# Kernel optimization log

Measured on AMD Instinct MI355X. Metric: run time of the kernel, lower is better.

## Reference

```python
import jax, jax.numpy as jnp
import numpy as np

B, M, S, N, DIN, C = 2048, 5, 128, 128, 64, 32
MID = C // 2  # 16
EPS = 1e-5
NEG_SLOPE = 0.2


def setup_inputs() -> dict:
    key = jax.random.key(0)
    ks = jax.random.split(key, 13)
    sc = lambda fan: 1.0 / np.sqrt(fan)
    return {
        "x_global": jax.random.normal(ks[0], (B, N, C), jnp.float32),
        "x_local": jax.random.normal(ks[1], (B * M, S, DIN), jnp.float32),
        "W_lin": jax.random.normal(ks[2], (C, DIN), jnp.float32) * sc(DIN),
        "b_lin": jnp.zeros((C,), jnp.float32),
        "W_att": jax.random.normal(ks[3], (C,), jnp.float32) * sc(C),  # Conv2d(C,1,1) weight
        "Wa": jax.random.normal(ks[4], (MID, C), jnp.float32) * sc(C),
        "Wb": jax.random.normal(ks[5], (MID, C), jnp.float32) * sc(C),
        "Wc": jax.random.normal(ks[6], (MID, C), jnp.float32) * sc(C),
        "Wn": jax.random.normal(ks[7], (MID, MID), jnp.float32) * sc(MID),
        "Wl": jax.random.normal(ks[8], (MID, MID), jnp.float32) * sc(MID),
        "Wd": jax.random.normal(ks[9], (C, 2 * MID), jnp.float32) * sc(2 * MID),
        "bn_gamma": jnp.ones((C,), jnp.float32),
        "bn_beta": jnp.zeros((C,), jnp.float32),
    }


def reference(x_global, x_local, W_lin, b_lin, W_att, Wa, Wb, Wc, Wn, Wl, Wd, bn_gamma, bn_beta):
    # --- Motion_Aggregation_Module.forward ---
    xl = x_local.reshape(B, M, S, DIN)
    xl = jnp.einsum('bmsd,cd->bmsc', xl, W_lin) + b_lin          # Linear(64,32)
    curves = jnp.transpose(xl, (0, 3, 1, 2))                      # [B,C,M,S]
    x = jnp.transpose(x_global, (0, 2, 1))                        # [B,C,N]

    # --- Correlation_Module.forward ---
    att = jnp.einsum('c,bcms->bms', W_att, curves)                # line_conv_att -> [B,M,S]
    inter = jnp.einsum('bcms,bms->bcm', curves, jax.nn.softmax(att, axis=-1))  # [B,C,M]
    intra = jnp.einsum('bcms,bms->bcs', curves, jax.nn.softmax(att, axis=-2))  # [B,C,S]

    inter = jnp.einsum('oc,bcm->bom', Wa, inter)                  # conva -> [B,MID,M]
    intra = jnp.einsum('oc,bcs->bos', Wb, intra)                  # convb -> [B,MID,S]
    x_logits = jnp.einsum('oc,bcn->bno', Wc, x)                   # convc^T -> [B,N,MID]

    a_inter = jax.nn.softmax(jnp.einsum('bno,bom->bnm', x_logits, inter), axis=-1)  # [B,N,M]
    a_intra = jax.nn.softmax(jnp.einsum('bno,bos->bns', x_logits, intra), axis=-1)  # [B,N,S]

    v_inter = jnp.einsum('po,bom->bmp', Wn, inter)                # convn^T -> [B,M,MID]
    v_intra = jnp.einsum('po,bos->bsp', Wl, intra)                # convl^T -> [B,S,MID]

    f_inter = jnp.einsum('bnm,bmp->bnp', a_inter, v_inter)        # [B,N,MID]
    f_intra = jnp.einsum('bns,bsp->bnp', a_intra, v_intra)        # [B,N,MID]
    feat = jnp.concatenate([f_inter, f_intra], axis=-1)           # [B,N,2*MID]
    feat = jnp.einsum('oc,bnc->bon', Wd, feat)                    # convd conv -> [B,C,N]

    # BatchNorm1d (training mode: batch stats over (B, N), biased variance)
    mean = feat.mean(axis=(0, 2), keepdims=True)
    var = feat.var(axis=(0, 2), keepdims=True)
    feat = (feat - mean) * jax.lax.rsqrt(var + EPS)
    feat = feat * bn_gamma[None, :, None] + bn_beta[None, :, None]

    out = x + feat                                                # residual
    out = jnp.where(out >= 0, out, NEG_SLOPE * out)               # leaky_relu(0.2)
    return jnp.transpose(out, (0, 2, 1))                          # [B,N,C]
```

## Files before the change

kernel.cpp:

```cpp
#include <hip/hip_runtime.h>
#include <math.h>

#define NB 2048
typedef float f32x4 __attribute__((ext_vector_type(4)));
typedef float f32x2 __attribute__((ext_vector_type(2)));

#define P_WAL 0
#define P_WBL 1024
#define P_WLBL 2048
#define P_WNAL 3072
#define P_WEFF 4096
#define P_BWA 4160
#define P_BWB 4176
#define P_BWL 4192
#define P_BWN 4208
#define P_C0  4224

#define WS_BNPART 4352
#define WS_COEF   135424
#define WS_SMALL  135488
#define WS_BIG_I  463168
#define WS_BIG_V  (463168 + 4194304)
#define WS_FEAT16 (463168 + 8388608)

__device__ __forceinline__ unsigned short f2bf(float f) {
  unsigned int u = __float_as_uint(f);
  u += 0x7fffu + ((u >> 16) & 1u);
  return (unsigned short)(u >> 16);
}
__device__ __forceinline__ unsigned int pack2bf(float lo, float hi) {
  return (unsigned int)f2bf(lo) | ((unsigned int)f2bf(hi) << 16);
}
__device__ __forceinline__ float bflo(unsigned int u) { return __uint_as_float(u << 16); }
__device__ __forceinline__ float bfhi(unsigned int u) { return __uint_as_float(u & 0xffff0000u); }

#define BSTAGE(MASK, HALF)                                        \
  { const bool hi_ = (lane & (MASK)) != 0;                        \
    _Pragma("unroll")                                             \
    for (int k_ = 0; k_ < (HALF); ++k_) {                         \
      float mine_ = hi_ ? a[k_ + (HALF)] : a[k_];                 \
      float oth_  = hi_ ? a[k_] : a[k_ + (HALF)];                 \
      a[k_] = mine_ + __shfl_xor(oth_, (MASK));                   \
    } }

__global__ __launch_bounds__(256) void k0_pre(const float* __restrict__ W_lin,
                                              const float* __restrict__ b_lin,
                                              const float* __restrict__ W_att,
                                              const float* __restrict__ Wa,
                                              const float* __restrict__ Wb,
                                              const float* __restrict__ Wn,
                                              const float* __restrict__ Wl,
                                              float* __restrict__ pre) {
  int t = threadIdx.x;
  for (int i = t; i < 1024; i += 256) {
    int o = i >> 6, d = i & 63;
    float sa = 0.f, sb = 0.f;
    for (int c = 0; c < 32; ++c) {
      float wl = W_lin[c * 64 + d];
      sa += Wa[o * 32 + c] * wl;
      sb += Wb[o * 32 + c] * wl;
    }
    pre[P_WAL + i] = sa;
    pre[P_WBL + i] = sb;
  }
  if (t < 64) {
    float s = 0.f;
    for (int c = 0; c < 32; ++c) s += W_att[c] * W_lin[c * 64 + t];
    pre[P_WEFF + t] = s;
  }
  if (t < 16) {
    float sa = 0.f, sb = 0.f;
    for (int c = 0; c < 32; ++c) {
      sa += Wa[t * 32 + c] * b_lin[c];
      sb += Wb[t * 32 + c] * b_lin[c];
    }
    pre[P_BWA + t] = sa;
    pre[P_BWB + t] = sb;
  }
  if (t == 0) {
    float s = 0.f;
    for (int c = 0; c < 32; ++c) s += W_att[c] * b_lin[c];
    pre[P_C0] = s;
  }
  __syncthreads();
  for (int i = t; i < 1024; i += 256) {
    int p_ = i >> 6, d = i & 63;
    float sl = 0.f, sn = 0.f;
    for (int o = 0; o < 16; ++o) {
      sl += Wl[p_ * 16 + o] * pre[P_WBL + o * 64 + d];
      sn += Wn[p_ * 16 + o] * pre[P_WAL + o * 64 + d];
    }
    pre[P_WLBL + i] = sl;
    pre[P_WNAL + i] = sn;
  }
  if (t < 16) {
    float sl = 0.f, sn = 0.f;
    for (int o = 0; o < 16; ++o) {
      sl += Wl[t * 16 + o] * pre[P_BWB + o];
      sn += Wn[t * 16 + o] * pre[P_BWA + o];
    }
    pre[P_BWL + t] = sl;
    pre[P_BWN + t] = sn;
  }
}

__global__ __launch_bounds__(1024, 2) void k1a(
    const float* __restrict__ xl_all, const float* __restrict__ pre,
    float* __restrict__ p_small, float* __restrict__ bigI,
    float* __restrict__ bigV) {
  __shared__ __align__(16) float xaggi[128 * 68];
  __shared__ f32x4 scratch5[5][16][16];
  __shared__ float pe[5][16];
  __shared__ float xagg_inter[5][64];

  const int t = threadIdx.x;
  const int b = blockIdx.x;
  const int lane = t & 63;
  const int w = t >> 6;
  const int q = lane >> 4;
  const int i16 = lane & 15;

  const float* xl = xl_all + (size_t)b * (5 * 128 * 64);
  const f32x4 weff4 = ((const f32x4*)(pre + P_WEFF))[i16];
  const float c0 = pre[P_C0];

  const float* xb = xl + (size_t)(8 * w + q) * 64 + 4 * i16;

  f32x4 xA[2], xB[2], acc[2];
  float Zk[2];
  #pragma unroll
  for (int k = 0; k < 2; ++k) {
    acc[k] = (f32x4)0.f;
    Zk[k] = 0.f;
    xA[k] = *(const f32x4*)(xb + k * 256);
  }

  #pragma unroll
  for (int m = 0; m < 5; ++m) {
    f32x4* xc = (m & 1) ? xB : xA;
    f32x4* xn = (m & 1) ? xA : xB;
    if (m < 4) {
      const float* np = xb + (size_t)(m + 1) * 8192;
      #pragma unroll
      for (int k = 0; k < 2; ++k) xn[k] = *(const f32x4*)(np + k * 256);
    }
    float a0, a1;
    {
      f32x4 p0 = xc[0] * weff4, p1 = xc[1] * weff4;
      a0 = p0.x + p0.y + p0.z + p0.w;
      a1 = p1.x + p1.y + p1.z + p1.w;
    }
    #pragma unroll
    for (int mask = 1; mask <= 8; mask <<= 1) {
      a0 += __shfl_xor(a0, mask);
      a1 += __shfl_xor(a1, mask);
    }
    float e0 = __expf(a0 + c0), e1 = __expf(a1 + c0);
    Zk[0] += e0; Zk[1] += e1;
    f32x4 pim;
    {
      f32x4 pr0 = e0 * xc[0];
      f32x4 pr1 = e1 * xc[1];
      acc[0] += pr0; acc[1] += pr1;
      pim = pr0 + pr1;
    }
    float se = e0 + e1;
    #pragma unroll
    for (int mask = 16; mask <= 32; mask <<= 1) {
      pim.x += __shfl_xor(pim.x, mask);
      pim.y += __shfl_xor(pim.y, mask);
      pim.z += __shfl_xor(pim.z, mask);
      pim.w += __shfl_xor(pim.w, mask);
      se += __shfl_xor(se, mask);
    }
    if (lane < 16) {
      scratch5[m][w][i16] = pim;
      if (i16 == 0) pe[m][w] = se;
    }
  }

  #pragma unroll
  for (int k = 0; k < 2; ++k) {
    float invz = 1.f / Zk[k];
    f32x4 v = acc[k] * invz;
    int r = 8 * w + 4 * k + q;
    *(f32x4*)&xaggi[r * 68 + 4 * i16] = v;
  }
  __syncthreads();

  if (t < 320) {
    int mm = t >> 6, d = t & 63;
    const float* sp = (const float*)&scratch5[mm][0][0];
    float s = 0.f;
    #pragma unroll
    for (int j = 0; j < 16; ++j) s += sp[j * 64 + d];
    float sume = 0.f;
    #pragma unroll
    for (int j = 0; j < 16; ++j) sume += pe[mm][j];
    xagg_inter[mm][d] = s / sume;
  }
  __syncthreads();

  if (t < 512) {
    const int q2 = __builtin_amdgcn_readfirstlane(t >> 7);
    const int s2 = t & 127;
    const float* Wbase = pre + ((q2 < 2) ? P_WBL : P_WLBL) + (q2 & 1) * 512;
    const float* xrow = &xaggi[s2 * 68];
    float acc2[8];
    #pragma unroll
    for (int r = 0; r < 8; ++r) acc2[r] = 0.f;
    #pragma unroll
    for (int c = 0; c < 64; c += 4) {
      f32x4 xa = *(const f32x4*)(xrow + c);
      #pragma unroll
      for (int r = 0; r < 8; ++r)
        acc2[r] += xa.x * Wbase[r * 64 + c] + xa.y * Wbase[r * 64 + c + 1] +
                   xa.z * Wbase[r * 64 + c + 2] + xa.w * Wbase[r * 64 + c + 3];
    }
    const int bb = ((q2 < 2) ? P_BWB : P_BWL) + (q2 & 1) * 8;
    float* dst = ((q2 < 2) ? bigI : bigV) + (size_t)b * 2048 + s2 * 16 + (q2 & 1) * 8;
    f32x4 o0, o1;
    o0.x = acc2[0] + pre[bb + 0];
    o0.y = acc2[1] + pre[bb + 1];
    o0.z = acc2[2] + pre[bb + 2];
    o0.w = acc2[3] + pre[bb + 3];
    o1.x = acc2[4] + pre[bb + 4];
    o1.y = acc2[5] + pre[bb + 5];
    o1.z = acc2[6] + pre[bb + 6];
    o1.w = acc2[7] + pre[bb + 7];
    *(f32x4*)dst = o0;
    *(f32x4*)(dst + 4) = o1;
  } else if (t < 672) {
    int tt = t - 512;
    int o2 = tt & 31, mm = tt >> 5;
    const float* wr = pre + ((o2 < 16) ? (P_WAL + o2 * 64) : (P_WNAL + (o2 - 16) * 64));
    float p = 0.f;
    #pragma unroll
    for (int d = 0; d < 64; ++d) p += wr[d] * xagg_inter[mm][d];
    p += (o2 < 16) ? pre[P_BWA + o2] : pre[P_BWN + (o2 - 16)];
    float* os = p_small + (size_t)b * 160;
    if (o2 < 16) os[mm * 16 + o2] = p;
    else os[80 + mm * 16 + (o2 - 16)] = p;
  }
}

__global__ __launch_bounds__(256, 4) void k1b(
    const float* __restrict__ xg_all, const float* __restrict__ Wc_g,
    const float* __restrict__ Wd_g, const float* __restrict__ p_small,
    const float* __restrict__ bigI, const float* __restrict__ bigV,
    unsigned int* __restrict__ feat16, float* __restrict__ bn_part) {
  __shared__ __align__(16) float UN[10240];
  float* slabI = UN;
  float* slabV = UN + 2560;
  float* xlogL = UN + 5120;
  __shared__ float s_sm[160];
  __shared__ float part1[2][32];
  __shared__ float part2[2][32];

  const int t = threadIdx.x;
  const int b = blockIdx.x;
  const int lane = t & 63;
  const int w = t >> 6;

  {
    const f32x4* gI = (const f32x4*)(bigI + (size_t)b * 2048);
    const f32x4* gV = (const f32x4*)(bigV + (size_t)b * 2048);
    #pragma unroll
    for (int j = 0; j < 2; ++j) {
      int idx = t + 256 * j;
      int row = idx >> 2, c4 = idx & 3;
      *(f32x4*)&slabI[row * 20 + 4 * c4] = gI[idx];
      *(f32x4*)&slabV[row * 20 + 4 * c4] = gV[idx];
    }
  }
  if (t < 128) {
    const int n = t;
    const f32x4* xgr = (const f32x4*)(xg_all + ((size_t)b * 128 + n) * 32);
    f32x4 xv[8];
    #pragma unroll
    for (int j = 0; j < 8; ++j) xv[j] = xgr[j];
    #pragma unroll
    for (int o4 = 0; o4 < 4; ++o4) {
      f32x4 r;
      #pragma unroll
      for (int jj = 0; jj < 4; ++jj) {
        const int o = o4 * 4 + jj;
        f32x4 s = (f32x4)0.f;
        #pragma unroll
        for (int j = 0; j < 8; ++j) s += xv[j] * *(const f32x4*)(Wc_g + o * 32 + 4 * j);
        r[jj] = s.x + s.y + s.z + s.w;
      }
      *(f32x4*)&xlogL[n * 20 + 4 * o4] = r;
    }
  }
  if (t >= 96) {
    int i2 = t - 96;
    s_sm[i2] = p_small[(size_t)b * 160 + i2];
  }
  __syncthreads();

  const int n0 = lane, n1 = lane + 64;
  f32x4 xlg0[4], xlg1[4];
  #pragma unroll
  for (int c = 0; c < 4; ++c) {
    xlg0[c] = *(const f32x4*)&xlogL[n0 * 20 + 4 * c];
    xlg1[c] = *(const f32x4*)&xlogL[n1 * 20 + 4 * c];
  }

  float s0 = 0.f, s1 = 0.f;
  f32x4 fav0[4], fav1[4];
  #pragma unroll
  for (int c = 0; c < 4; ++c) { fav0[c] = (f32x4)0.f; fav1[c] = (f32x4)0.f; }
  for (int k = 0; k < 32; ++k) {
    const int i = 32 * w + k;
    const f32x4* rI = (const f32x4*)&slabI[i * 20];
    f32x4 d0 = xlg0[0] * rI[0] + xlg0[1] * rI[1] + xlg0[2] * rI[2] + xlg0[3] * rI[3];
    f32x4 d1 = xlg1[0] * rI[0] + xlg1[1] * rI[1] + xlg1[2] * rI[2] + xlg1[3] * rI[3];
    float e0 = __expf(d0.x + d0.y + d0.z + d0.w);
    float e1 = __expf(d1.x + d1.y + d1.z + d1.w);
    s0 += e0; s1 += e1;
    const f32x4* rV = (const f32x4*)&slabV[i * 20];
    #pragma unroll
    for (int c = 0; c < 4; ++c) {
      f32x4 v = rV[c];
      fav0[c] += e0 * v;
      fav1[c] += e1 * v;
    }
  }
  __syncthreads();

  {
    float* c0p = UN + w * 2560 + n0 * 20;
    float* c1p = UN + w * 2560 + n1 * 20;
    #pragma unroll
    for (int c = 0; c < 4; ++c) {
      *(f32x4*)&c0p[4 * c] = fav0[c];
      *(f32x4*)&c1p[4 * c] = fav1[c];
    }
    c0p[16] = s0;
    c1p[16] = s1;
  }
  __syncthreads();

  {
    const int n = t & 127, g = t >> 7;
    if (g == 0) {
      f32x4 a0 = (f32x4)0.f, a1 = (f32x4)0.f;
      #pragma unroll
      for (int ww = 0; ww < 4; ++ww) {
        const float* cp = UN + ww * 2560 + n * 20;
        a0 += *(const f32x4*)&cp[0];
        a1 += *(const f32x4*)&cp[4];
      }
      float* dp = UN + n * 20;
      *(f32x4*)&dp[0] = a0;
      *(f32x4*)&dp[4] = a1;
    } else {
      f32x4 a2 = (f32x4)0.f, a3 = (f32x4)0.f;
      float as = 0.f;
      #pragma unroll
      for (int ww = 0; ww < 4; ++ww) {
        const float* cp = UN + ww * 2560 + n * 20;
        a2 += *(const f32x4*)&cp[8];
        a3 += *(const f32x4*)&cp[12];
        as += cp[16];
      }
      float* dp = UN + n * 20;
      *(f32x4*)&dp[8] = a2;
      *(f32x4*)&dp[12] = a3;
      dp[16] = as;
    }
  }
  __syncthreads();

  if (t < 128) {
    const int n = t;
    const float* cp = UN + n * 20;
    f32x4 fav[4];
    #pragma unroll
    for (int c = 0; c < 4; ++c) fav[c] = *(const f32x4*)&cp[4 * c];
    const float inv = 1.f / cp[16];
    f32x4 fin[4];
    #pragma unroll
    for (int c = 0; c < 4; ++c) fin[c] = fav[c] * inv;

    f32x4 xme[4];
    #pragma unroll
    for (int c = 0; c < 4; ++c) xme[c] = (t < 64) ? xlg0[c] : xlg1[c];

    float L[5], mx3 = -1e30f;
    #pragma unroll
    for (int mm = 0; mm < 5; ++mm) {
      float p = 0.f;
      #pragma unroll
      for (int c = 0; c < 4; ++c) {
        #pragma unroll
        for (int jj = 0; jj < 4; ++jj) p += xme[c][jj] * s_sm[mm * 16 + 4 * c + jj];
      }
      L[mm] = p;
      mx3 = fmaxf(mx3, p);
    }
    float sum3 = 0.f;
    #pragma unroll
    for (int mm = 0; mm < 5; ++mm) { L[mm] = __expf(L[mm] - mx3); sum3 += L[mm]; }
    const float inv3 = 1.f / sum3;
    f32x4 fi[4];
    #pragma unroll
    for (int o4 = 0; o4 < 4; ++o4) {
      f32x4 r;
      #pragma unroll
      for (int jj = 0; jj < 4; ++jj) {
        float p = 0.f;
        #pragma unroll
        for (int mm = 0; mm < 5; ++mm) p += L[mm] * s_sm[80 + mm * 16 + o4 * 4 + jj];
        r[jj] = p * inv3;
      }
      fi[o4] = r;
    }

    f32x4 feat[8];
    #pragma unroll
    for (int o4 = 0; o4 < 8; ++o4) {
      f32x4 r;
      #pragma unroll
      for (int jj = 0; jj < 4; ++jj) {
        const int o = o4 * 4 + jj;
        f32x4 s = (f32x4)0.f;
        #pragma unroll
        for (int j = 0; j < 4; ++j) {
          s += fi[j]  * *(const f32x4*)(Wd_g + o * 32 + 4 * j);
          s += fin[j] * *(const f32x4*)(Wd_g + o * 32 + 16 + 4 * j);
        }
        r[jj] = s.x + s.y + s.z + s.w;
      }
      feat[o4] = r;
    }
    {
      unsigned int* op = feat16 + ((size_t)b * 128 + n) * 16;
      uint4 u0, u1, u2, u3;
      u0.x = pack2bf(feat[0].x, feat[0].y); u0.y = pack2bf(feat[0].z, feat[0].w);
      u0.z = pack2bf(feat[1].x, feat[1].y); u0.w = pack2bf(feat[1].z, feat[1].w);
      u1.x = pack2bf(feat[2].x, feat[2].y); u1.y = pack2bf(feat[2].z, feat[2].w);
      u1.z = pack2bf(feat[3].x, feat[3].y); u1.w = pack2bf(feat[3].z, feat[3].w);
      u2.x = pack2bf(feat[4].x, feat[4].y); u2.y = pack2bf(feat[4].z, feat[4].w);
      u2.z = pack2bf(feat[5].x, feat[5].y); u2.w = pack2bf(feat[5].z, feat[5].w);
      u3.x = pack2bf(feat[6].x, feat[6].y); u3.y = pack2bf(feat[6].z, feat[6].w);
      u3.z = pack2bf(feat[7].x, feat[7].y); u3.w = pack2bf(feat[7].z, feat[7].w);
      ((uint4*)op)[0] = u0;
      ((uint4*)op)[1] = u1;
      ((uint4*)op)[2] = u2;
      ((uint4*)op)[3] = u3;
    }

    const int w2 = t >> 6;
    const int kmap = ((lane & 1) << 4) | ((lane & 2) << 2) | (lane & 4) |
                     ((lane >> 2) & 2) | ((lane >> 4) & 1);
    {
      float a[32];
      #pragma unroll
      for (int o = 0; o < 32; ++o) a[o] = feat[o >> 2][o & 3];
      BSTAGE(1, 16) BSTAGE(2, 8) BSTAGE(4, 4) BSTAGE(8, 2) BSTAGE(16, 1)
      a[0] += __shfl_xor(a[0], 32);
      if (lane < 32) part1[w2][kmap] = a[0];
    }
    {
      float a[32];
      #pragma unroll
      for (int o = 0; o < 32; ++o) { float v = feat[o >> 2][o & 3]; a[o] = v * v; }
      BSTAGE(1, 16) BSTAGE(2, 8) BSTAGE(4, 4) BSTAGE(8, 2) BSTAGE(16, 1)
      a[0] += __shfl_xor(a[0], 32);
      if (lane < 32) part2[w2][kmap] = a[0];
    }
  }
  __syncthreads();
  if (t < 64) {
    int c = t & 31, h = t >> 5;
    float v = h ? (part2[0][c] + part2[1][c]) : (part1[0][c] + part1[1][c]);
    bn_part[(size_t)b * 64 + h * 32 + c] = v;
  }
}

__global__ __launch_bounds__(256, 1) void k2_stats(const float* __restrict__ bn_part,
                                                   const float* __restrict__ gamma,
                                                   const float* __restrict__ beta,
                                                   float* __restrict__ coef) {
  __shared__ float red[2][4];
  const int c = blockIdx.x;
  const int t = threadIdx.x;
  const int lane = t & 63, w = t >> 6;
  float s1 = 0.f, s2 = 0.f;
  for (int bb = t; bb < NB; bb += 256) {
    s1 += bn_part[(size_t)bb * 64 + c];
    s2 += bn_part[(size_t)bb * 64 + c + 32];
  }
  #pragma unroll
  for (int mask = 1; mask <= 32; mask <<= 1) {
    s1 += __shfl_xor(s1, mask);
    s2 += __shfl_xor(s2, mask);
  }
  if (lane == 0) { red[0][w] = s1; red[1][w] = s2; }
  __syncthreads();
  if (t == 0) {
    float S1 = red[0][0] + red[0][1] + red[0][2] + red[0][3];
    float S2 = red[1][0] + red[1][1] + red[1][2] + red[1][3];
    const float inv = 1.f / (float)(NB * 128);
    float mean = S1 * inv;
    float var = S2 * inv - mean * mean;
    float scl = gamma[c] * rsqrtf(var + 1e-5f);
    coef[c] = scl;
    coef[32 + c] = beta[c] - mean * scl;
  }
}

__global__ __launch_bounds__(256) void k3_final(const float* __restrict__ xg,
                                                const unsigned int* __restrict__ feat16,
                                                float* __restrict__ out,
                                                const float* __restrict__ coef) {
  __shared__ float s_c[64];
  if (threadIdx.x < 64) s_c[threadIdx.x] = coef[threadIdx.x];
  __syncthreads();
  size_t i4 = (size_t)blockIdx.x * 256 + threadIdx.x;
  uint2 fu = ((const uint2*)feat16)[i4];
  float4 x = ((const float4*)xg)[i4];
  int c = (int)((i4 * 4) & 31);
  float4 r;
  r.x = x.x + bflo(fu.x) * s_c[c + 0] + s_c[32 + c + 0];
  r.y = x.y + bfhi(fu.x) * s_c[c + 1] + s_c[32 + c + 1];
  r.z = x.z + bflo(fu.y) * s_c[c + 2] + s_c[32 + c + 2];
  r.w = x.w + bfhi(fu.y) * s_c[c + 3] + s_c[32 + c + 3];
  r.x = r.x >= 0.f ? r.x : 0.2f * r.x;
  r.y = r.y >= 0.f ? r.y : 0.2f * r.y;
  r.z = r.z >= 0.f ? r.z : 0.2f * r.z;
  r.w = r.w >= 0.f ? r.w : 0.2f * r.w;
  ((float4*)out)[i4] = r;
}

extern "C" void kernel_launch(void* const* d_in, const int* in_sizes, int n_in,
                              void* d_out, int out_size, void* d_ws, size_t ws_size,
                              hipStream_t stream) {
  const float* xg    = (const float*)d_in[0];
  const float* xl    = (const float*)d_in[1];
  const float* W_lin = (const float*)d_in[2];
  const float* b_lin = (const float*)d_in[3];
  const float* W_att = (const float*)d_in[4];
  const float* Wa    = (const float*)d_in[5];
  const float* Wb    = (const float*)d_in[6];
  const float* Wc    = (const float*)d_in[7];
  const float* Wn    = (const float*)d_in[8];
  const float* Wl    = (const float*)d_in[9];
  const float* Wd    = (const float*)d_in[10];
  const float* gamma = (const float*)d_in[11];
  const float* beta  = (const float*)d_in[12];
  float* out = (float*)d_out;
  float* ws = (float*)d_ws;
  float* pre = ws;
  float* bn_part = ws + WS_BNPART;
  float* coef = ws + WS_COEF;
  float* p_small = ws + WS_SMALL;
  float* bigI = ws + WS_BIG_I;
  float* bigV = ws + WS_BIG_V;
  unsigned int* feat16 = (unsigned int*)(ws + WS_FEAT16);

  hipLaunchKernelGGL(k0_pre, dim3(1), dim3(256), 0, stream,
                     W_lin, b_lin, W_att, Wa, Wb, Wn, Wl, pre);
  hipLaunchKernelGGL(k1a, dim3(NB), dim3(1024), 0, stream, xl, pre, p_small, bigI, bigV);
  hipLaunchKernelGGL(k1b, dim3(NB), dim3(256), 0, stream,
                     xg, Wc, Wd, p_small, bigI, bigV, feat16, bn_part);
  hipLaunchKernelGGL(k2_stats, dim3(32), dim3(256), 0, stream, bn_part, gamma, beta, coef);
  hipLaunchKernelGGL(k3_final, dim3(8192), dim3(256), 0, stream, xg, feat16, out, coef);
}
```

Baseline: 195.9 us.

## Compute intra attention in k1b with bf16 MFMA matrix instructions

Replaces the scalar FP32 per-thread loop for the intra attention (x_logits × I, exp, then × V) with bf16 MFMA 16x16x32 tiles. The exp-probability matrix is staged in shared memory as bf16 so it can feed a second MFMA against transposed V. This drops the cross-wave partial reduction through shared memory. It lowers precision of the logits, probabilities and V to bf16, uses more LDS, and halves the occupancy hint in launch bounds.

```diff
diff --git a/kernel.cpp b/kernel.cpp
--- a/kernel.cpp
+++ b/kernel.cpp
@@ -4,6 +4,7 @@
 #define NB 2048
 typedef float f32x4 __attribute__((ext_vector_type(4)));
 typedef float f32x2 __attribute__((ext_vector_type(2)));
+typedef short s16x8 __attribute__((ext_vector_type(8)));
 
 #define P_WAL 0
 #define P_WBL 1024
@@ -244,15 +245,16 @@
   }
 }
 
-__global__ __launch_bounds__(256, 4) void k1b(
+__global__ __launch_bounds__(256, 2) void k1b(
     const float* __restrict__ xg_all, const float* __restrict__ Wc_g,
     const float* __restrict__ Wd_g, const float* __restrict__ p_small,
     const float* __restrict__ bigI, const float* __restrict__ bigV,
     unsigned int* __restrict__ feat16, float* __restrict__ bn_part) {
-  __shared__ __align__(16) float UN[10240];
-  float* slabI = UN;
-  float* slabV = UN + 2560;
-  float* xlogL = UN + 5120;
+  __shared__ __align__(16) unsigned short slabI_[128 * 40];
+  __shared__ __align__(16) unsigned short xlogB_[128 * 40];
+  __shared__ __align__(16) unsigned short VT_[16 * 148];
+  __shared__ __align__(16) unsigned short Pm_[128 * 148];
+  __shared__ __align__(16) float finL_[128 * 20];
   __shared__ float s_sm[160];
   __shared__ float part1[2][32];
   __shared__ float part2[2][32];
@@ -261,17 +263,39 @@
   const int b = blockIdx.x;
   const int lane = t & 63;
   const int w = t >> 6;
+  const int r = lane & 15;
+  const int g = lane >> 4;
 
   {
     const f32x4* gI = (const f32x4*)(bigI + (size_t)b * 2048);
-    const f32x4* gV = (const f32x4*)(bigV + (size_t)b * 2048);
     #pragma unroll
     for (int j = 0; j < 2; ++j) {
       int idx = t + 256 * j;
       int row = idx >> 2, c4 = idx & 3;
-      *(f32x4*)&slabI[row * 20 + 4 * c4] = gI[idx];
-      *(f32x4*)&slabV[row * 20 + 4 * c4] = gV[idx];
-    }
+      f32x4 v = gI[idx];
+      unsigned int* dst = (unsigned int*)&slabI_[row * 40 + c4 * 4];
+      dst[0] = pack2bf(v.x, v.y);
+      dst[1] = pack2bf(v.z, v.w);
+    }
+  }
+  for (int i = t; i < 1024; i += 256) {
+    int row = i >> 3, c = i & 7;
+    ((unsigned int*)slabI_)[row * 20 + 8 + c] = 0u;
+    ((unsigned int*)xlogB_)[row * 20 + 8 + c] = 0u;
+  }
+  {
+    const f32x4* gV = (const f32x4*)(bigV + (size_t)b * 2048);
+    int s = t >> 1, ph = (t & 1) * 8;
+    f32x4 v0 = gV[t * 2];
+    f32x4 v1 = gV[t * 2 + 1];
+    VT_[(ph + 0) * 148 + s] = f2bf(v0.x);
+    VT_[(ph + 1) * 148 + s] = f2bf(v0.y);
+    VT_[(ph + 2) * 148 + s] = f2bf(v0.z);
+    VT_[(ph + 3) * 148 + s] = f2bf(v0.w);
+    VT_[(ph + 4) * 148 + s] = f2bf(v1.x);
+    VT_[(ph + 5) * 148 + s] = f2bf(v1.y);
+    VT_[(ph + 6) * 148 + s] = f2bf(v1.z);
+    VT_[(ph + 7) * 148 + s] = f2bf(v1.w);
   }
   if (t < 128) {
     const int n = t;
@@ -279,19 +303,29 @@
     f32x4 xv[8];
     #pragma unroll
     for (int j = 0; j < 8; ++j) xv[j] = xgr[j];
-    #pragma unroll
-    for (int o4 = 0; o4 < 4; ++o4) {
-      f32x4 r;
-      #pragma unroll
-      for (int jj = 0; jj < 4; ++jj) {
-        const int o = o4 * 4 + jj;
+    unsigned int px[8];
+    #pragma unroll
+    for (int o2 = 0; o2 < 8; ++o2) {
+      float v0, v1;
+      {
+        const int o = o2 * 2;
         f32x4 s = (f32x4)0.f;
         #pragma unroll
         for (int j = 0; j < 8; ++j) s += xv[j] * *(const f32x4*)(Wc_g + o * 32 + 4 * j);
-        r[jj] = s.x + s.y + s.z + s.w;
-      }
-      *(f32x4*)&xlogL[n * 20 + 4 * o4] = r;
-    }
+        v0 = s.x + s.y + s.z + s.w;
+      }
+      {
+        const int o = o2 * 2 + 1;
+        f32x4 s = (f32x4)0.f;
+        #pragma unroll
+        for (int j = 0; j < 8; ++j) s += xv[j] * *(const f32x4*)(Wc_g + o * 32 + 4 * j);
+        v1 = s.x + s.y + s.z + s.w;
+      }
+      px[o2] = pack2bf(v0, v1);
+    }
+    unsigned int* dst = (unsigned int*)&xlogB_[n * 40];
+    ((uint4*)dst)[0] = make_uint4(px[0], px[1], px[2], px[3]);
+    ((uint4*)dst)[1] = make_uint4(px[4], px[5], px[6], px[7]);
   }
   if (t >= 96) {
     int i2 = t - 96;
@@ -299,95 +333,84 @@
   }
   __syncthreads();
 
-  const int n0 = lane, n1 = lane + 64;
-  f32x4 xlg0[4], xlg1[4];
+  float inv_rs[2][4];
   #pragma unroll
-  for (int c = 0; c < 4; ++c) {
-    xlg0[c] = *(const f32x4*)&xlogL[n0 * 20 + 4 * c];
-    xlg1[c] = *(const f32x4*)&xlogL[n1 * 20 + 4 * c];
-  }
-
-  float s0 = 0.f, s1 = 0.f;
-  f32x4 fav0[4], fav1[4];
+  for (int h = 0; h < 2; ++h) {
+    const int nt = 2 * w + h;
+    s16x8 afr = *(const s16x8*)&xlogB_[(nt * 16 + r) * 40 + g * 8];
+    f32x4 d[8];
+    #pragma unroll
+    for (int st = 0; st < 8; ++st) {
+      s16x8 bfr = *(const s16x8*)&slabI_[(st * 16 + r) * 40 + g * 8];
+      d[st] = __builtin_amdgcn_mfma_f32_16x16x32_bf16(afr, bfr, (f32x4)0.f, 0, 0, 0);
+    }
+    float rs[4] = {0.f, 0.f, 0.f, 0.f};
+    #pragma unroll
+    for (int st = 0; st < 8; ++st) {
+      #pragma unroll
+      for (int j = 0; j < 4; ++j) {
+        float e = __expf(d[st][j]);
+        rs[j] += e;
+        Pm_[(nt * 16 + g * 4 + j) * 148 + st * 16 + r] = f2bf(e);
+      }
+    }
+    #pragma unroll
+    for (int j = 0; j < 4; ++j) {
+      rs[j] += __shfl_xor(rs[j], 1);
+      rs[j] += __shfl_xor(rs[j], 2);
+      rs[j] += __shfl_xor(rs[j], 4);
+      rs[j] += __shfl_xor(rs[j], 8);
+      inv_rs[h][j] = 1.f / rs[j];
+    }
+  }
+
   #pragma unroll
-  for (int c = 0; c < 4; ++c) { fav0[c] = (f32x4)0.f; fav1[c] = (f32x4)0.f; }
-  for (int k = 0; k < 32; ++k) {
-    const int i = 32 * w + k;
-    const f32x4* rI = (const f32x4*)&slabI[i * 20];
-    f32x4 d0 = xlg0[0] * rI[0] + xlg0[1] * rI[1] + xlg0[2] * rI[2] + xlg0[3] * rI[3];
-    f32x4 d1 = xlg1[0] * rI[0] + xlg1[1] * rI[1] + xlg1[2] * rI[2] + xlg1[3] * rI[3];
-    float e0 = __expf(d0.x + d0.y + d0.z + d0.w);
-    float e1 = __expf(d1.x + d1.y + d1.z + d1.w);
-    s0 += e0; s1 += e1;
-    const f32x4* rV = (const f32x4*)&slabV[i * 20];
-    #pragma unroll
-    for (int c = 0; c < 4; ++c) {
-      f32x4 v = rV[c];
-      fav0[c] += e0 * v;
-      fav1[c] += e1 * v;
-    }
-  }
-  __syncthreads();
-
-  {
-    float* c0p = UN + w * 2560 + n0 * 20;
-    float* c1p = UN + w * 2560 + n1 * 20;
-    #pragma unroll
-    for (int c = 0; c < 4; ++c) {
-      *(f32x4*)&c0p[4 * c] = fav0[c];
-      *(f32x4*)&c1p[4 * c] = fav1[c];
-    }
-    c0p[16] = s0;
-    c1p[16] = s1;
-  }
-  __syncthreads();
-
-  {
-    const int n = t & 127, g = t >> 7;
-    if (g == 0) {
-      f32x4 a0 = (f32x4)0.f, a1 = (f32x4)0.f;
-      #pragma unroll
-      for (int ww = 0; ww < 4; ++ww) {
-        const float* cp = UN + ww * 2560 + n * 20;
-        a0 += *(const f32x4*)&cp[0];
-        a1 += *(const f32x4*)&cp[4];
-      }
-      float* dp = UN + n * 20;
-      *(f32x4*)&dp[0] = a0;
-      *(f32x4*)&dp[4] = a1;
-    } else {
-      f32x4 a2 = (f32x4)0.f, a3 = (f32x4)0.f;
-      float as = 0.f;
-      #pragma unroll
-      for (int ww = 0; ww < 4; ++ww) {
-        const float* cp = UN + ww * 2560 + n * 20;
-        a2 += *(const f32x4*)&cp[8];
-        a3 += *(const f32x4*)&cp[12];
-        as += cp[16];
-      }
-      float* dp = UN + n * 20;
-      *(f32x4*)&dp[8] = a2;
-      *(f32x4*)&dp[12] = a3;
-      dp[16] = as;
-    }
+  for (int h = 0; h < 2; ++h) {
+    const int nt = 2 * w + h;
+    f32x4 c = (f32x4)0.f;
+    const unsigned int* Pu = (const unsigned int*)Pm_;
+    const unsigned int* Vu = (const unsigned int*)VT_;
+    #pragma unroll
+    for (int kt = 0; kt < 4; ++kt) {
+      s16x8 afr, bfr;
+      {
+        int base = (nt * 16 + r) * 74 + kt * 16 + g * 4;
+        uint2 a0 = *(const uint2*)&Pu[base];
+        uint2 a1 = *(const uint2*)&Pu[base + 2];
+        ((uint2*)&afr)[0] = a0;
+        ((uint2*)&afr)[1] = a1;
+      }
+      {
+        int base = r * 74 + kt * 16 + g * 4;
+        uint2 b0 = *(const uint2*)&Vu[base];
+        uint2 b1 = *(const uint2*)&Vu[base + 2];
+        ((uint2*)&bfr)[0] = b0;
+        ((uint2*)&bfr)[1] = b1;
+      }
+      c = __builtin_amdgcn_mfma_f32_16x16x32_bf16(afr, bfr, c, 0, 0, 0);
+    }
+    #pragma unroll
+    for (int j = 0; j < 4; ++j)
+      finL_[(nt * 16 + g * 4 + j) * 20 + r] = c[j] * inv_rs[h][j];
   }
   __syncthreads();
 
   if (t < 128) {
     const int n = t;
-    const float* cp = UN + n * 20;
-    f32x4 fav[4];
-    #pragma unroll
-    for (int c = 0; c < 4; ++c) fav[c] = *(const f32x4*)&cp[4 * c];
-    const float inv = 1.f / cp[16];
     f32x4 fin[4];
     #pragma unroll
-    for (int c = 0; c < 4; ++c) fin[c] = fav[c] * inv;
-
+    for (int c = 0; c < 4; ++c) fin[c] = *(const f32x4*)&finL_[n * 20 + 4 * c];
     f32x4 xme[4];
-    #pragma unroll
-    for (int c = 0; c < 4; ++c) xme[c] = (t < 64) ? xlg0[c] : xlg1[c];
-
+    {
+      const unsigned int* src = (const unsigned int*)&xlogB_[n * 40];
+      #pragma unroll
+      for (int c = 0; c < 4; ++c) {
+        unsigned int u0 = src[2 * c], u1 = src[2 * c + 1];
+        f32x4 v;
+        v.x = bflo(u0); v.y = bfhi(u0); v.z = bflo(u1); v.w = bfhi(u1);
+        xme[c] = v;
+      }
+    }
     float L[5], mx3 = -1e30f;
     #pragma unroll
     for (int mm = 0; mm < 5; ++mm) {
@@ -407,21 +430,20 @@
     f32x4 fi[4];
     #pragma unroll
     for (int o4 = 0; o4 < 4; ++o4) {
-      f32x4 r;
+      f32x4 rr;
       #pragma unroll
       for (int jj = 0; jj < 4; ++jj) {
         float p = 0.f;
         #pragma unroll
         for (int mm = 0; mm < 5; ++mm) p += L[mm] * s_sm[80 + mm * 16 + o4 * 4 + jj];
-        r[jj] = p * inv3;
-      }
-      fi[o4] = r;
-    }
-
+        rr[jj] = p * inv3;
+      }
+      fi[o4] = rr;
+    }
     f32x4 feat[8];
     #pragma unroll
     for (int o4 = 0; o4 < 8; ++o4) {
-      f32x4 r;
+      f32x4 rr;
       #pragma unroll
       for (int jj = 0; jj < 4; ++jj) {
         const int o = o4 * 4 + jj;
@@ -431,9 +453,9 @@
           s += fi[j]  * *(const f32x4*)(Wd_g + o * 32 + 4 * j);
           s += fin[j] * *(const f32x4*)(Wd_g + o * 32 + 16 + 4 * j);
         }
-        r[jj] = s.x + s.y + s.z + s.w;
-      }
-      feat[o4] = r;
+        rr[jj] = s.x + s.y + s.z + s.w;
+      }
+      feat[o4] = rr;
     }
     {
       unsigned int* op = feat16 + ((size_t)b * 128 + n) * 16;
@@ -451,7 +473,6 @@
       ((uint4*)op)[2] = u2;
       ((uint4*)op)[3] = u3;
     }
-
     const int w2 = t >> 6;
     const int kmap = ((lane & 1) << 4) | ((lane & 2) << 2) | (lane & 4) |
                      ((lane >> 2) & 2) | ((lane >> 4) & 1);
```

New measurement: 191.0 us. 1.03x faster.
